# Optimization experiments

Hardware: AMD Instinct MI355X
Metric: run time of the kernel (lower is better)

The kernel has to match this reference:

```python
import jax, jax.numpy as jnp
import numpy as np

N = 100000
E = 1200000
F_IN = 128
HID = 32
HEADS = 4
OUT_HEADS = 1
N_CLASSES = 40
NEG_SLOPE = 0.2


def _glorot(key, shape):
    fan_in, fan_out = shape[0], shape[-1]
    lim = jnp.sqrt(6.0 / (fan_in + fan_out))
    return jax.random.uniform(key, shape, jnp.float32, -lim, lim)


def setup_inputs() -> dict:
    key = jax.random.key(0)
    ks = jax.random.split(key, 16)
    x = jax.random.normal(ks[0], (N, F_IN), jnp.float32)
    edge_index = jax.random.randint(ks[1], (2, E), 0, N, jnp.int32)
    # layer 0: F_IN -> HID per head, HEADS heads, concat
    W0 = _glorot(ks[2], (F_IN, HEADS * HID))
    a_src0 = _glorot(ks[3], (HEADS, HID))
    a_dst0 = _glorot(ks[4], (HEADS, HID))
    b0 = jnp.zeros((HEADS * HID,), jnp.float32)
    # layer 1: HEADS*HID -> HID per head, HEADS heads, concat
    W1 = _glorot(ks[5], (HEADS * HID, HEADS * HID))
    a_src1 = _glorot(ks[6], (HEADS, HID))
    a_dst1 = _glorot(ks[7], (HEADS, HID))
    b1 = jnp.zeros((HEADS * HID,), jnp.float32)
    # layer 2: HEADS*HID -> N_CLASSES, OUT_HEADS heads, concat=False (mean)
    W2 = _glorot(ks[8], (HEADS * HID, OUT_HEADS * N_CLASSES))
    a_src2 = _glorot(ks[9], (OUT_HEADS, N_CLASSES))
    a_dst2 = _glorot(ks[10], (OUT_HEADS, N_CLASSES))
    b2 = jnp.zeros((N_CLASSES,), jnp.float32)
    return dict(x=x, edge_index=edge_index,
                W0=W0, a_src0=a_src0, a_dst0=a_dst0, b0=b0,
                W1=W1, a_src1=a_src1, a_dst1=a_dst1, b1=b1,
                W2=W2, a_src2=a_src2, a_dst2=a_dst2, b2=b2)


def gat_conv(x, src, dst, W, a_src, a_dst, b, heads, ch, concat):
    n = x.shape[0]
    h = (x @ W).reshape(n, heads, ch)                      # [N,H,C]
    # per-node attention logits for source/target roles
    s_src = jnp.einsum('nhc,hc->nh', h, a_src)             # [N,H]
    s_dst = jnp.einsum('nhc,hc->nh', h, a_dst)             # [N,H]
    e = jax.nn.leaky_relu(s_src[src] + s_dst[dst], NEG_SLOPE)  # [E,H]
    # segment softmax over incoming edges of each target node
    emax = jax.ops.segment_max(e, dst, num_segments=n)
    ex = jnp.exp(e - emax[dst])
    denom = jax.ops.segment_sum(ex, dst, num_segments=n)
    alpha = ex / (denom[dst] + 1e-16)                       # [E,H]
    msg = h[src] * alpha[:, :, None]                        # [E,H,C]
    out = jax.ops.segment_sum(msg, dst, num_segments=n)     # [N,H,C]
    out = out.reshape(n, heads * ch) if concat else out.mean(axis=1)
    return out + b


def reference(x, edge_index, W0, a_src0, a_dst0, b0, W1, a_src1, a_dst1, b1,
              W2, a_src2, a_dst2, b2):
    # add self loops (PyG GATConv default)
    loops = jnp.arange(N, dtype=edge_index.dtype)
    src = jnp.concatenate([edge_index[0], loops])
    dst = jnp.concatenate([edge_index[1], loops])
    h = jax.nn.elu(gat_conv(x, src, dst, W0, a_src0, a_dst0, b0, HEADS, HID, True))
    h = jax.nn.elu(gat_conv(h, src, dst, W1, a_src1, a_dst1, b1, HEADS, HID, True))
    h = gat_conv(h, src, dst, W2, a_src2, a_dst2, b2, OUT_HEADS, N_CLASSES, False)
    return jax.nn.log_softmax(h, axis=1)
```

## Files before the change

kernel.cpp:

```cpp
#include <hip/hip_runtime.h>
#include <hip/hip_bf16.h>

#define FIN   128
#define HEADS 4
#define HID   32
#define NCLS  40
#define NEG_SLOPE 0.2f

#define BKT_SH 10
#define BKT    1024
#define NB_MAX 128
#define TILE_E 8192

typedef __bf16 bf16x8 __attribute__((ext_vector_type(8)));
typedef float  f32x4  __attribute__((ext_vector_type(4)));

__device__ inline unsigned short bf16_rne(float f) {
    unsigned u = __float_as_uint(f);
    return (unsigned short)((u + 0x7fffu + ((u >> 16) & 1u)) >> 16);
}
__device__ inline float bf16_to_f(unsigned short h) {
    return __uint_as_float(((unsigned)h) << 16);
}

__device__ inline void packW_dev(const float* __restrict__ W, unsigned short* __restrict__ Bhi,
                                 unsigned short* __restrict__ Blo, int NO, int NC, int idx) {
    int i = idx & 7;
    int rest = idx >> 3;
    int l = rest & 63;
    int rest2 = rest >> 6;
    int c = rest2 % NC;
    int t = rest2 / NC;
    int k   = t * 32 + (l >> 4) * 8 + i;
    int col = c * 16 + (l & 15);
    float val = (col < NO) ? W[(size_t)k * NO + col] : 0.f;
    unsigned short hi = bf16_rne(val);
    unsigned short lo = bf16_rne(val - bf16_to_f(hi));
    Bhi[idx] = hi;
    Blo[idx] = lo;
}

__device__ inline void packS_dev(const float* __restrict__ W, const float* __restrict__ asrc,
                                 const float* __restrict__ adst, unsigned short* __restrict__ Shi,
                                 unsigned short* __restrict__ Slo, int NO, int HH, int CH, int idx) {
    int i = idx & 7;
    int l = (idx >> 3) & 63;
    int t = idx >> 9;
    int k = t * 32 + (l >> 4) * 8 + i;
    int j = l & 15;
    float val = 0.f;
    if (j < 2 * HH) {
        int h = (j < HH) ? j : j - HH;
        const float* av = (j < HH) ? (asrc + h * CH) : (adst + h * CH);
        const float* wr = W + (size_t)k * NO + h * CH;
        for (int c = 0; c < CH; ++c) val += wr[c] * av[c];
    }
    unsigned short hi = bf16_rne(val);
    unsigned short lo = bf16_rne(val - bf16_to_f(hi));
    Shi[idx] = hi;
    Slo[idx] = lo;
}

__global__ __launch_bounds__(256) void packAll_k(
        const float* __restrict__ W0, const float* __restrict__ W1, const float* __restrict__ W2,
        const float* __restrict__ as0, const float* __restrict__ ad0,
        const float* __restrict__ as1, const float* __restrict__ ad1,
        const float* __restrict__ as2, const float* __restrict__ ad2,
        unsigned short* __restrict__ Bhi0, unsigned short* __restrict__ Blo0,
        unsigned short* __restrict__ Bhi1, unsigned short* __restrict__ Blo1,
        unsigned short* __restrict__ Bhi2, unsigned short* __restrict__ Blo2,
        unsigned short* __restrict__ Shi0, unsigned short* __restrict__ Slo0,
        unsigned short* __restrict__ Shi1, unsigned short* __restrict__ Slo1,
        unsigned short* __restrict__ Shi2, unsigned short* __restrict__ Slo2,
        int* __restrict__ cnt1) {
    int gid = blockIdx.x * 256 + threadIdx.x;
    if      (gid < 16384) packW_dev(W0, Bhi0, Blo0, 128, 8, gid);
    else if (gid < 32768) packW_dev(W1, Bhi1, Blo1, 128, 8, gid - 16384);
    else if (gid < 38912) packW_dev(W2, Bhi2, Blo2, NCLS, 3, gid - 32768);
    else if (gid < 40960) packS_dev(W0, as0, ad0, Shi0, Slo0, 128, 4, HID, gid - 38912);
    else if (gid < 43008) packS_dev(W1, as1, ad1, Shi1, Slo1, 128, 4, HID, gid - 40960);
    else if (gid < 45056) packS_dev(W2, as2, ad2, Shi2, Slo2, NCLS, 1, NCLS, gid - 43008);
    else if (gid < 45056 + NB_MAX) cnt1[gid - 45056] = 0;
}

template<int NC, int HH>
__global__ __launch_bounds__(256) void gemm_fused_k(
        const float* __restrict__ X, const unsigned short* __restrict__ Bhi,
        const unsigned short* __restrict__ Blo, const unsigned short* __restrict__ Shi,
        const unsigned short* __restrict__ Slo, unsigned short* __restrict__ Hbf,
        float* __restrict__ ssrc, float* __restrict__ sdst, int n, int NO) {
    int wave = threadIdx.x >> 6;
    int lane = threadIdx.x & 63;
    int rowbase = (blockIdx.x * 4 + wave) * 32;
    if (rowbase >= n) return;
    int r0 = lane & 15, kg = lane >> 4;

    f32x4 acc[2][NC];
    f32x4 accS[2];
#pragma unroll
    for (int rt = 0; rt < 2; ++rt) {
        accS[rt] = f32x4{0.f, 0.f, 0.f, 0.f};
#pragma unroll
        for (int c = 0; c < NC; ++c) acc[rt][c] = f32x4{0.f, 0.f, 0.f, 0.f};
    }

    for (int t = 0; t < 4; ++t) {
        union U { unsigned short u[8]; bf16x8 v; };
        U ah[2], al[2];
#pragma unroll
        for (int rt = 0; rt < 2; ++rt) {
            int row = min(rowbase + rt * 16 + r0, n - 1);
            const float* xp = X + (size_t)row * 128 + t * 32 + kg * 8;
            float4 xa = *reinterpret_cast<const float4*>(xp);
            float4 xb = *reinterpret_cast<const float4*>(xp + 4);
            float f[8] = {xa.x, xa.y, xa.z, xa.w, xb.x, xb.y, xb.z, xb.w};
#pragma unroll
            for (int i = 0; i < 8; ++i) {
                unsigned short h = bf16_rne(f[i]);
                ah[rt].u[i] = h;
                al[rt].u[i] = bf16_rne(f[i] - bf16_to_f(h));
            }
        }
#pragma unroll
        for (int c = 0; c < NC; ++c) {
            size_t boff = (((size_t)t * NC + c) * 64 + lane) * 8;
            bf16x8 bh = *reinterpret_cast<const bf16x8*>(Bhi + boff);
            bf16x8 bl = *reinterpret_cast<const bf16x8*>(Blo + boff);
#pragma unroll
            for (int rt = 0; rt < 2; ++rt) {
                acc[rt][c] = __builtin_amdgcn_mfma_f32_16x16x32_bf16(ah[rt].v, bh, acc[rt][c], 0, 0, 0);
                acc[rt][c] = __builtin_amdgcn_mfma_f32_16x16x32_bf16(al[rt].v, bh, acc[rt][c], 0, 0, 0);
                acc[rt][c] = __builtin_amdgcn_mfma_f32_16x16x32_bf16(ah[rt].v, bl, acc[rt][c], 0, 0, 0);
            }
        }
        {
            size_t soff = ((size_t)t * 64 + lane) * 8;
            bf16x8 sh = *reinterpret_cast<const bf16x8*>(Shi + soff);
            bf16x8 sl = *reinterpret_cast<const bf16x8*>(Slo + soff);
#pragma unroll
            for (int rt = 0; rt < 2; ++rt) {
                accS[rt] = __builtin_amdgcn_mfma_f32_16x16x32_bf16(ah[rt].v, sh, accS[rt], 0, 0, 0);
                accS[rt] = __builtin_amdgcn_mfma_f32_16x16x32_bf16(al[rt].v, sh, accS[rt], 0, 0, 0);
                accS[rt] = __builtin_amdgcn_mfma_f32_16x16x32_bf16(ah[rt].v, sl, accS[rt], 0, 0, 0);
            }
        }
    }

#pragma unroll
    for (int rt = 0; rt < 2; ++rt)
#pragma unroll
        for (int r = 0; r < 4; ++r) {
            int row = rowbase + rt * 16 + kg * 4 + r;
            if (row >= n) continue;
            if (HH == 4) {
                if (r0 < 4)      ssrc[(size_t)row * 4 + r0]       = accS[rt][r];
                else if (r0 < 8) sdst[(size_t)row * 4 + (r0 - 4)] = accS[rt][r];
            } else {
                if (r0 == 0)      ssrc[row] = accS[rt][r];
                else if (r0 == 1) sdst[row] = accS[rt][r];
            }
#pragma unroll
            for (int c = 0; c < NC; ++c) {
                int col = c * 16 + r0;
                if (col < NO)
                    Hbf[(size_t)row * NO + col] = bf16_rne(acc[rt][c][r]);
            }
        }
}

template<int NC, int HH, bool SPLIT>
__global__ __launch_bounds__(256) void gemm_bf16s_k(
        const unsigned short* __restrict__ Xbf, const unsigned short* __restrict__ Bhi,
        const unsigned short* __restrict__ Blo, const unsigned short* __restrict__ Shi,
        const unsigned short* __restrict__ Slo, unsigned short* __restrict__ Hbf,
        unsigned short* __restrict__ H8,
        float* __restrict__ ssrc, float* __restrict__ sdst, int n, int NO) {
    int wave = threadIdx.x >> 6;
    int lane = threadIdx.x & 63;
    int rowbase = (blockIdx.x * 4 + wave) * 32;
    if (rowbase >= n) return;
    int r0 = lane & 15, kg = lane >> 4;

    f32x4 acc[2][NC];
    f32x4 accS[2];
#pragma unroll
    for (int rt = 0; rt < 2; ++rt) {
        accS[rt] = f32x4{0.f, 0.f, 0.f, 0.f};
#pragma unroll
        for (int c = 0; c < NC; ++c) acc[rt][c] = f32x4{0.f, 0.f, 0.f, 0.f};
    }

    for (int t = 0; t < 4; ++t) {
        bf16x8 av[2];
#pragma unroll
        for (int rt = 0; rt < 2; ++rt) {
            int row = min(rowbase + rt * 16 + r0, n - 1);
            av[rt] = *reinterpret_cast<const bf16x8*>(Xbf + (size_t)row * 128 + t * 32 + kg * 8);
        }
#pragma unroll
        for (int c = 0; c < NC; ++c) {
            size_t boff = (((size_t)t * NC + c) * 64 + lane) * 8;
            bf16x8 bh = *reinterpret_cast<const bf16x8*>(Bhi + boff);
            bf16x8 bl = *reinterpret_cast<const bf16x8*>(Blo + boff);
#pragma unroll
            for (int rt = 0; rt < 2; ++rt) {
                acc[rt][c] = __builtin_amdgcn_mfma_f32_16x16x32_bf16(av[rt], bh, acc[rt][c], 0, 0, 0);
                acc[rt][c] = __builtin_amdgcn_mfma_f32_16x16x32_bf16(av[rt], bl, acc[rt][c], 0, 0, 0);
            }
        }
        {
            size_t soff = ((size_t)t * 64 + lane) * 8;
            bf16x8 sh = *reinterpret_cast<const bf16x8*>(Shi + soff);
            bf16x8 sl = *reinterpret_cast<const bf16x8*>(Slo + soff);
#pragma unroll
            for (int rt = 0; rt < 2; ++rt) {
                accS[rt] = __builtin_amdgcn_mfma_f32_16x16x32_bf16(av[rt], sh, accS[rt], 0, 0, 0);
                accS[rt] = __builtin_amdgcn_mfma_f32_16x16x32_bf16(av[rt], sl, accS[rt], 0, 0, 0);
            }
        }
    }

#pragma unroll
    for (int rt = 0; rt < 2; ++rt)
#pragma unroll
        for (int r = 0; r < 4; ++r) {
            int row = rowbase + rt * 16 + kg * 4 + r;
            if (row >= n) continue;
            if (HH == 4) {
                if (r0 < 4)      ssrc[(size_t)row * 4 + r0]       = accS[rt][r];
                else if (r0 < 8) sdst[(size_t)row * 4 + (r0 - 4)] = accS[rt][r];
            } else {
                if (r0 == 0)      ssrc[row] = accS[rt][r];
                else if (r0 == 1) sdst[row] = accS[rt][r];
            }
#pragma unroll
            for (int c = 0; c < NC; ++c) {
                int col = c * 16 + r0;
                if (col < NO) {
                    unsigned short b = bf16_rne(acc[rt][c][r]);
                    if (!SPLIT) {
                        Hbf[(size_t)row * 128 + col] = b;
                    } else {
                        if (col < 32) Hbf[(size_t)row * 32 + col] = b;
                        else          H8[(size_t)row * 8 + (col - 32)] = b;
                    }
                }
            }
        }
}

__global__ __launch_bounds__(256) void histA_k(const int* __restrict__ ei, int E, int Etot,
                                               int nb, int* __restrict__ cnt1) {
    __shared__ int h[NB_MAX];
    for (int i = threadIdx.x; i < nb; i += 256) h[i] = 0;
    __syncthreads();
    int base = blockIdx.x * TILE_E;
    int lim = min(base + TILE_E, Etot);
    for (int e = base + threadIdx.x; e < lim; e += 256) {
        int d = (e < E) ? ei[E + e] : e - E;
        atomicAdd(&h[d >> BKT_SH], 1);
    }
    __syncthreads();
    for (int i = threadIdx.x; i < nb; i += 256)
        if (h[i]) atomicAdd(&cnt1[i], h[i]);
}

__global__ void scanB_k(const int* __restrict__ cnt1, int* __restrict__ bbase,
                        int* __restrict__ gcur1, int nb) {
    __shared__ int tmp[128];
    int l = threadIdx.x;
    int v = (l < nb) ? cnt1[l] : 0;
    tmp[l] = v;
    __syncthreads();
    for (int off = 1; off < 128; off <<= 1) {
        int t = (l >= off) ? tmp[l - off] : 0;
        __syncthreads();
        tmp[l] += t;
        __syncthreads();
    }
    if (l < nb) { int ex = tmp[l] - v; bbase[l] = ex; gcur1[l] = ex; }
    if (l == 0) bbase[nb] = tmp[127];
}

__global__ __launch_bounds__(256) void placeA_k(const int* __restrict__ ei, int E, int Etot,
                                                int nb, int* __restrict__ gcur1,
                                                unsigned* __restrict__ pairs) {
    __shared__ int h[NB_MAX];
    __shared__ int cur[NB_MAX];
    for (int i = threadIdx.x; i < nb; i += 256) h[i] = 0;
    __syncthreads();
    int base = blockIdx.x * TILE_E;
    int lim = min(base + TILE_E, Etot);
    for (int e = base + threadIdx.x; e < lim; e += 256) {
        int d = (e < E) ? ei[E + e] : e - E;
        atomicAdd(&h[d >> BKT_SH], 1);
    }
    __syncthreads();
    for (int i = threadIdx.x; i < nb; i += 256)
        cur[i] = h[i] ? atomicAdd(&gcur1[i], h[i]) : 0;
    __syncthreads();
    for (int e = base + threadIdx.x; e < lim; e += 256) {
        int s, d;
        if (e < E) { s = ei[e]; d = ei[E + e]; } else { s = d = e - E; }
        int p = atomicAdd(&cur[d >> BKT_SH], 1);
        pairs[p] = ((unsigned)s << BKT_SH) | (unsigned)(d & (BKT - 1));
    }
}

__global__ __launch_bounds__(256) void buildcsr_k(const unsigned* __restrict__ pairs,
                                                  const int* __restrict__ bbase,
                                                  int* __restrict__ rowptr,
                                                  int* __restrict__ cols,
                                                  int n, int etot) {
    __shared__ int cnt[BKT];
    __shared__ int part[256];
    int b = blockIdx.x;
    int d0 = b << BKT_SH;
    int nd = min(BKT, n - d0);
    int rbeg = bbase[b], rend = bbase[b + 1];
    for (int i = threadIdx.x; i < nd; i += 256) cnt[i] = 0;
    __syncthreads();
    for (int i = rbeg + threadIdx.x; i < rend; i += 256)
        atomicAdd(&cnt[pairs[i] & (BKT - 1)], 1);
    __syncthreads();

    int t = threadIdx.x;
    int i4 = t * 4;
    int myv[4];
    int s0 = 0;
#pragma unroll
    for (int j = 0; j < 4; ++j) { myv[j] = (i4 + j < nd) ? cnt[i4 + j] : 0; s0 += myv[j]; }
    part[t] = s0;
    __syncthreads();
    for (int off = 1; off < 256; off <<= 1) {
        int tv = (t >= off) ? part[t - off] : 0;
        __syncthreads();
        part[t] += tv;
        __syncthreads();
    }
    int run = rbeg + part[t] - s0;
#pragma unroll
    for (int j = 0; j < 4; ++j) {
        if (i4 + j < nd) {
            rowptr[d0 + i4 + j] = run;
            cnt[i4 + j] = run;
            run += myv[j];
        }
    }
    if (b == 0 && t == 0) rowptr[n] = etot;
    __syncthreads();
    for (int i = rbeg + threadIdx.x; i < rend; i += 256) {
        unsigned p = pairs[i];
        int pos = atomicAdd(&cnt[p & (BKT - 1)], 1);
        cols[pos] = (int)(p >> BKT_SH);
    }
}

__global__ __launch_bounds__(256) void gat128_k(
        const int* __restrict__ rp, const int* __restrict__ cols,
        const unsigned short* __restrict__ Hbf, const float* __restrict__ ssrc,
        const float* __restrict__ sdst, const float* __restrict__ bias,
        unsigned short* __restrict__ outbf, int n) {
    int d = (blockIdx.x * 256 + threadIdx.x) >> 4;
    if (d >= n) return;
    int l = threadIdx.x & 15;
    int head = l >> 2;
    int beg = rp[d], end = rp[d + 1];

    float sdh = sdst[(size_t)d * 4 + head];

    float4 a0 = {0.f, 0.f, 0.f, 0.f}, a1 = {0.f, 0.f, 0.f, 0.f};
    float4 c0 = {0.f, 0.f, 0.f, 0.f}, c1 = {0.f, 0.f, 0.f, 0.f};
    float den = 0.f;

    auto proc = [&](int i, float4& p0, float4& p1) {
        int s = cols[i];
        float v = ssrc[(size_t)s * 4 + head] + sdh;
        v = (v >= 0.f) ? v : NEG_SLOPE * v;
        float a = __expf(v);
        den += a;
        const unsigned short* hp = Hbf + (size_t)s * 128 + l * 8;
        uint4 q = *reinterpret_cast<const uint4*>(hp);
        p0.x += a * __uint_as_float(q.x << 16);
        p0.y += a * __uint_as_float(q.x & 0xffff0000u);
        p0.z += a * __uint_as_float(q.y << 16);
        p0.w += a * __uint_as_float(q.y & 0xffff0000u);
        p1.x += a * __uint_as_float(q.z << 16);
        p1.y += a * __uint_as_float(q.z & 0xffff0000u);
        p1.z += a * __uint_as_float(q.w << 16);
        p1.w += a * __uint_as_float(q.w & 0xffff0000u);
    };

    int i = beg;
    int rem = (end - beg) & 3;
    if (rem & 1) { proc(i, a0, a1); ++i; }
    if (rem & 2) { proc(i, a0, a1); proc(i + 1, c0, c1); i += 2; }
    for (; i < end; i += 4) {
        int s0 = cols[i], s1 = cols[i + 1], s2 = cols[i + 2], s3 = cols[i + 3];
        float w0 = ssrc[(size_t)s0 * 4 + head] + sdh;
        float w1 = ssrc[(size_t)s1 * 4 + head] + sdh;
        float w2 = ssrc[(size_t)s2 * 4 + head] + sdh;
        float w3 = ssrc[(size_t)s3 * 4 + head] + sdh;
        uint4 q0 = *reinterpret_cast<const uint4*>(Hbf + (size_t)s0 * 128 + l * 8);
        uint4 q1 = *reinterpret_cast<const uint4*>(Hbf + (size_t)s1 * 128 + l * 8);
        uint4 q2 = *reinterpret_cast<const uint4*>(Hbf + (size_t)s2 * 128 + l * 8);
        uint4 q3 = *reinterpret_cast<const uint4*>(Hbf + (size_t)s3 * 128 + l * 8);
        w0 = (w0 >= 0.f) ? w0 : NEG_SLOPE * w0;
        w1 = (w1 >= 0.f) ? w1 : NEG_SLOPE * w1;
        w2 = (w2 >= 0.f) ? w2 : NEG_SLOPE * w2;
        w3 = (w3 >= 0.f) ? w3 : NEG_SLOPE * w3;
        float e0 = __expf(w0), e1 = __expf(w1);
        float e2 = __expf(w2), e3 = __expf(w3);
        den += e0 + e1 + e2 + e3;
        a0.x += e0 * __uint_as_float(q0.x << 16);
        a0.y += e0 * __uint_as_float(q0.x & 0xffff0000u);
        a0.z += e0 * __uint_as_float(q0.y << 16);
        a0.w += e0 * __uint_as_float(q0.y & 0xffff0000u);
        a1.x += e0 * __uint_as_float(q0.z << 16);
        a1.y += e0 * __uint_as_float(q0.z & 0xffff0000u);
        a1.z += e0 * __uint_as_float(q0.w << 16);
        a1.w += e0 * __uint_as_float(q0.w & 0xffff0000u);
        c0.x += e1 * __uint_as_float(q1.x << 16);
        c0.y += e1 * __uint_as_float(q1.x & 0xffff0000u);
        c0.z += e1 * __uint_as_float(q1.y << 16);
        c0.w += e1 * __uint_as_float(q1.y & 0xffff0000u);
        c1.x += e1 * __uint_as_float(q1.z << 16);
        c1.y += e1 * __uint_as_float(q1.z & 0xffff0000u);
        c1.z += e1 * __uint_as_float(q1.w << 16);
        c1.w += e1 * __uint_as_float(q1.w & 0xffff0000u);
        a0.x += e2 * __uint_as_float(q2.x << 16);
        a0.y += e2 * __uint_as_float(q2.x & 0xffff0000u);
        a0.z += e2 * __uint_as_float(q2.y << 16);
        a0.w += e2 * __uint_as_float(q2.y & 0xffff0000u);
        a1.x += e2 * __uint_as_float(q2.z << 16);
        a1.y += e2 * __uint_as_float(q2.z & 0xffff0000u);
        a1.z += e2 * __uint_as_float(q2.w << 16);
        a1.w += e2 * __uint_as_float(q2.w & 0xffff0000u);
        c0.x += e3 * __uint_as_float(q3.x << 16);
        c0.y += e3 * __uint_as_float(q3.x & 0xffff0000u);
        c0.z += e3 * __uint_as_float(q3.y << 16);
        c0.w += e3 * __uint_as_float(q3.y & 0xffff0000u);
        c1.x += e3 * __uint_as_float(q3.z << 16);
        c1.y += e3 * __uint_as_float(q3.z & 0xffff0000u);
        c1.z += e3 * __uint_as_float(q3.w << 16);
        c1.w += e3 * __uint_as_float(q3.w & 0xffff0000u);
    }
    a0.x += c0.x; a0.y += c0.y; a0.z += c0.z; a0.w += c0.w;
    a1.x += c1.x; a1.y += c1.y; a1.z += c1.z; a1.w += c1.w;

    float r = 1.f / (den + 1e-16f);
    float4 b0 = *reinterpret_cast<const float4*>(bias + l * 8);
    float4 b1 = *reinterpret_cast<const float4*>(bias + l * 8 + 4);
    float4 v0, v1;
    v0.x = a0.x * r + b0.x; v0.y = a0.y * r + b0.y;
    v0.z = a0.z * r + b0.z; v0.w = a0.w * r + b0.w;
    v1.x = a1.x * r + b1.x; v1.y = a1.y * r + b1.y;
    v1.z = a1.z * r + b1.z; v1.w = a1.w * r + b1.w;
    v0.x = (v0.x > 0.f) ? v0.x : expm1f(v0.x);
    v0.y = (v0.y > 0.f) ? v0.y : expm1f(v0.y);
    v0.z = (v0.z > 0.f) ? v0.z : expm1f(v0.z);
    v0.w = (v0.w > 0.f) ? v0.w : expm1f(v0.w);
    v1.x = (v1.x > 0.f) ? v1.x : expm1f(v1.x);
    v1.y = (v1.y > 0.f) ? v1.y : expm1f(v1.y);
    v1.z = (v1.z > 0.f) ? v1.z : expm1f(v1.z);
    v1.w = (v1.w > 0.f) ? v1.w : expm1f(v1.w);

    uint4 u;
    u.x = (unsigned)bf16_rne(v0.x) | ((unsigned)bf16_rne(v0.y) << 16);
    u.y = (unsigned)bf16_rne(v0.z) | ((unsigned)bf16_rne(v0.w) << 16);
    u.z = (unsigned)bf16_rne(v1.x) | ((unsigned)bf16_rne(v1.y) << 16);
    u.w = (unsigned)bf16_rne(v1.z) | ((unsigned)bf16_rne(v1.w) << 16);
    *reinterpret_cast<uint4*>(outbf + (size_t)d * 128 + l * 8) = u;
}

__global__ __launch_bounds__(256) void gat40_k(
        const int* __restrict__ rp, const int* __restrict__ cols,
        const unsigned short* __restrict__ H32, const unsigned short* __restrict__ H8,
        const float* __restrict__ ssrc, const float* __restrict__ sdst,
        const float* __restrict__ b2, float* __restrict__ out, int n) {
    int d = (blockIdx.x * 256 + threadIdx.x) >> 4;
    if (d >= n) return;
    int l = threadIdx.x & 15;
    int beg = rp[d], end = rp[d + 1];
    float sd = sdst[d];

    bool lo32 = (l < 8);
    int o32 = l * 4;
    int o8  = ((l >= 8 && l < 10) ? (l - 8) : 0) * 4;

    float4 acc = {0.f, 0.f, 0.f, 0.f};
    float4 acc2 = {0.f, 0.f, 0.f, 0.f};
    float den = 0.f;

    auto proc = [&](int i, float4& p) {
        int s = cols[i];
        float v = ssrc[s] + sd;
        v = (v >= 0.f) ? v : NEG_SLOPE * v;
        float a = __expf(v);
        den += a;
        const unsigned short* hp = lo32 ? (H32 + (size_t)s * 32 + o32)
                                        : (H8  + (size_t)s * 8  + o8);
        uint2 q = *reinterpret_cast<const uint2*>(hp);
        p.x += a * __uint_as_float(q.x << 16);
        p.y += a * __uint_as_float(q.x & 0xffff0000u);
        p.z += a * __uint_as_float(q.y << 16);
        p.w += a * __uint_as_float(q.y & 0xffff0000u);
    };
    int i = beg;
    int rem = (end - beg) & 3;
    if (rem & 1) { proc(i, acc); ++i; }
    if (rem & 2) { proc(i, acc); proc(i + 1, acc2); i += 2; }
    for (; i < end; i += 4) {
        int s0 = cols[i], s1 = cols[i + 1], s2 = cols[i + 2], s3 = cols[i + 3];
        float w0 = ssrc[s0] + sd, w1 = ssrc[s1] + sd;
        float w2 = ssrc[s2] + sd, w3 = ssrc[s3] + sd;
        const unsigned short* p0 = lo32 ? (H32 + (size_t)s0 * 32 + o32) : (H8 + (size_t)s0 * 8 + o8);
        const unsigned short* p1 = lo32 ? (H32 + (size_t)s1 * 32 + o32) : (H8 + (size_t)s1 * 8 + o8);
        const unsigned short* p2 = lo32 ? (H32 + (size_t)s2 * 32 + o32) : (H8 + (size_t)s2 * 8 + o8);
        const unsigned short* p3 = lo32 ? (H32 + (size_t)s3 * 32 + o32) : (H8 + (size_t)s3 * 8 + o8);
        uint2 q0 = *reinterpret_cast<const uint2*>(p0);
        uint2 q1 = *reinterpret_cast<const uint2*>(p1);
        uint2 q2 = *reinterpret_cast<const uint2*>(p2);
        uint2 q3 = *reinterpret_cast<const uint2*>(p3);
        w0 = (w0 >= 0.f) ? w0 : NEG_SLOPE * w0;
        w1 = (w1 >= 0.f) ? w1 : NEG_SLOPE * w1;
        w2 = (w2 >= 0.f) ? w2 : NEG_SLOPE * w2;
        w3 = (w3 >= 0.f) ? w3 : NEG_SLOPE * w3;
        float e0 = __expf(w0), e1 = __expf(w1);
        float e2 = __expf(w2), e3 = __expf(w3);
        den += e0 + e1 + e2 + e3;
        acc.x += e0 * __uint_as_float(q0.x << 16);
        acc.y += e0 * __uint_as_float(q0.x & 0xffff0000u);
        acc.z += e0 * __uint_as_float(q0.y << 16);
        acc.w += e0 * __uint_as_float(q0.y & 0xffff0000u);
        acc2.x += e1 * __uint_as_float(q1.x << 16);
        acc2.y += e1 * __uint_as_float(q1.x & 0xffff0000u);
        acc2.z += e1 * __uint_as_float(q1.y << 16);
        acc2.w += e1 * __uint_as_float(q1.y & 0xffff0000u);
        acc.x += e2 * __uint_as_float(q2.x << 16);
        acc.y += e2 * __uint_as_float(q2.x & 0xffff0000u);
        acc.z += e2 * __uint_as_float(q2.y << 16);
        acc.w += e2 * __uint_as_float(q2.y & 0xffff0000u);
        acc2.x += e3 * __uint_as_float(q3.x << 16);
        acc2.y += e3 * __uint_as_float(q3.x & 0xffff0000u);
        acc2.z += e3 * __uint_as_float(q3.y << 16);
        acc2.w += e3 * __uint_as_float(q3.y & 0xffff0000u);
    }
    acc.x += acc2.x; acc.y += acc2.y; acc.z += acc2.z; acc.w += acc2.w;

    float r = 1.f / (den + 1e-16f);
    float4 v4 = {0.f, 0.f, 0.f, 0.f};
    float mm = -1e30f;
    if (l < 10) {
        float4 b = *reinterpret_cast<const float4*>(b2 + l * 4);
        v4.x = acc.x * r + b.x; v4.y = acc.y * r + b.y;
        v4.z = acc.z * r + b.z; v4.w = acc.w * r + b.w;
        mm = fmaxf(fmaxf(v4.x, v4.y), fmaxf(v4.z, v4.w));
    }
    for (int off = 8; off > 0; off >>= 1) mm = fmaxf(mm, __shfl_xor(mm, off, 16));
    float ss = 0.f;
    if (l < 10)
        ss = __expf(v4.x - mm) + __expf(v4.y - mm) + __expf(v4.z - mm) + __expf(v4.w - mm);
    for (int off = 8; off > 0; off >>= 1) ss += __shfl_xor(ss, off, 16);
    float lse = mm + logf(ss);
    if (l < 10) {
        float4 o;
        o.x = v4.x - lse; o.y = v4.y - lse; o.z = v4.z - lse; o.w = v4.w - lse;
        *reinterpret_cast<float4*>(out + (size_t)d * 40 + l * 4) = o;
    }
}

static inline dim3 g1(long t) { return dim3((unsigned)((t + 255) / 256)); }

extern "C" void kernel_launch(void* const* d_in, const int* in_sizes, int n_in,
                              void* d_out, int out_size, void* d_ws, size_t ws_size,
                              hipStream_t stream) {
    const float* x      = (const float*)d_in[0];
    const int*   ei     = (const int*)d_in[1];
    const float* W0     = (const float*)d_in[2];
    const float* a_src0 = (const float*)d_in[3];
    const float* a_dst0 = (const float*)d_in[4];
    const float* b0     = (const float*)d_in[5];
    const float* W1     = (const float*)d_in[6];
    const float* a_src1 = (const float*)d_in[7];
    const float* a_dst1 = (const float*)d_in[8];
    const float* b1     = (const float*)d_in[9];
    const float* W2     = (const float*)d_in[10];
    const float* a_src2 = (const float*)d_in[11];
    const float* a_dst2 = (const float*)d_in[12];
    const float* b2     = (const float*)d_in[13];

    const int N    = in_sizes[0] / FIN;
    const int E    = in_sizes[1] / 2;
    const int Etot = E + N;
    const int NB   = (N + BKT - 1) / BKT;

    float* ws = (float*)d_ws;
    size_t o = 0;
    unsigned short* Hbf = (unsigned short*)(ws + o); o += (size_t)N * FIN / 2;
    unsigned short* Obf = (unsigned short*)(ws + o); o += (size_t)N * FIN / 2;
    unsigned short* H8  = (unsigned short*)(ws + o); o += (size_t)N * 4;
    float* ssrcA = ws + o; o += (size_t)N * HEADS;
    float* sdstA = ws + o; o += (size_t)N * HEADS;
    float* ssrcB = ws + o; o += (size_t)N * HEADS;
    float* sdstB = ws + o; o += (size_t)N * HEADS;
    int* cnt1   = (int*)(ws + o); o += NB_MAX;
    int* bbase  = (int*)(ws + o); o += NB_MAX + 2;
    int* gcur1  = (int*)(ws + o); o += NB_MAX;
    int* rowptr = (int*)(ws + o); o += N + 1;
    int* cols   = (int*)(ws + o); o += Etot;
    unsigned* pairs = (unsigned*)(ws + o); o += Etot;
    unsigned short* Bhi0 = (unsigned short*)(ws + o); o += 4 * 8 * 64 * 8 / 2;
    unsigned short* Blo0 = (unsigned short*)(ws + o); o += 4 * 8 * 64 * 8 / 2;
    unsigned short* Bhi1 = (unsigned short*)(ws + o); o += 4 * 8 * 64 * 8 / 2;
    unsigned short* Blo1 = (unsigned short*)(ws + o); o += 4 * 8 * 64 * 8 / 2;
    unsigned short* Bhi2 = (unsigned short*)(ws + o); o += 4 * 3 * 64 * 8 / 2;
    unsigned short* Blo2 = (unsigned short*)(ws + o); o += 4 * 3 * 64 * 8 / 2;
    unsigned short* Shi0 = (unsigned short*)(ws + o); o += 4 * 64 * 8 / 2;
    unsigned short* Slo0 = (unsigned short*)(ws + o); o += 4 * 64 * 8 / 2;
    unsigned short* Shi1 = (unsigned short*)(ws + o); o += 4 * 64 * 8 / 2;
    unsigned short* Slo1 = (unsigned short*)(ws + o); o += 4 * 64 * 8 / 2;
    unsigned short* Shi2 = (unsigned short*)(ws + o); o += 4 * 64 * 8 / 2;
    unsigned short* Slo2 = (unsigned short*)(ws + o); o += 4 * 64 * 8 / 2;

    const int gemmBlocks = (N + 127) / 128;
    const int grpBlocks  = (N * 16 + 255) / 256;
    const int eTiles     = (Etot + TILE_E - 1) / TILE_E;

    packAll_k<<<g1(45056 + NB_MAX), 256, 0, stream>>>(
        W0, W1, W2, a_src0, a_dst0, a_src1, a_dst1, a_src2, a_dst2,
        Bhi0, Blo0, Bhi1, Blo1, Bhi2, Blo2,
        Shi0, Slo0, Shi1, Slo1, Shi2, Slo2, cnt1);
    histA_k<<<eTiles, 256, 0, stream>>>(ei, E, Etot, NB, cnt1);
    scanB_k<<<1, 128, 0, stream>>>(cnt1, bbase, gcur1, NB);
    placeA_k<<<eTiles, 256, 0, stream>>>(ei, E, Etot, NB, gcur1, pairs);
    buildcsr_k<<<NB, 256, 0, stream>>>(pairs, bbase, rowptr, cols, N, Etot);

    gemm_fused_k<8, 4><<<gemmBlocks, 256, 0, stream>>>(x, Bhi0, Blo0, Shi0, Slo0, Hbf, ssrcA, sdstA, N, 128);
    gat128_k<<<grpBlocks, 256, 0, stream>>>(rowptr, cols, Hbf, ssrcA, sdstA, b0, Obf, N);

    gemm_bf16s_k<8, 4, false><<<gemmBlocks, 256, 0, stream>>>(Obf, Bhi1, Blo1, Shi1, Slo1, Hbf, nullptr, ssrcB, sdstB, N, 128);
    gat128_k<<<grpBlocks, 256, 0, stream>>>(rowptr, cols, Hbf, ssrcB, sdstB, b1, Obf, N);

    gemm_bf16s_k<3, 1, true><<<gemmBlocks, 256, 0, stream>>>(Obf, Bhi2, Blo2, Shi2, Slo2, Hbf, H8, ssrcA, sdstA, N, NCLS);
    gat40_k<<<grpBlocks, 256, 0, stream>>>(rowptr, cols, Hbf, H8, ssrcA, sdstA, b2, (float*)d_out, N);
}
```

Before: 311.7 us.

## Drop histogram pass with fixed-capacity buckets and degree-sort destination nodes

New measurement: 928.9 us. 2.98x slower.

```diff
diff --git a/kernel.cpp b/kernel.cpp
--- a/kernel.cpp
+++ b/kernel.cpp
@@ -11,6 +11,8 @@
 #define BKT    1024
 #define NB_MAX 128
 #define TILE_E 8192
+#define CAP_SH 14
+#define CAP    16384
 
 typedef __bf16 bf16x8 __attribute__((ext_vector_type(8)));
 typedef float  f32x4  __attribute__((ext_vector_type(4)));
@@ -72,7 +74,7 @@
         unsigned short* __restrict__ Shi0, unsigned short* __restrict__ Slo0,
         unsigned short* __restrict__ Shi1, unsigned short* __restrict__ Slo1,
         unsigned short* __restrict__ Shi2, unsigned short* __restrict__ Slo2,
-        int* __restrict__ cnt1) {
+        int* __restrict__ gcur1, int* __restrict__ degcnt) {
     int gid = blockIdx.x * 256 + threadIdx.x;
     if      (gid < 16384) packW_dev(W0, Bhi0, Blo0, 128, 8, gid);
     else if (gid < 32768) packW_dev(W1, Bhi1, Blo1, 128, 8, gid - 16384);
@@ -80,7 +82,8 @@
     else if (gid < 40960) packS_dev(W0, as0, ad0, Shi0, Slo0, 128, 4, HID, gid - 38912);
     else if (gid < 43008) packS_dev(W1, as1, ad1, Shi1, Slo1, 128, 4, HID, gid - 40960);
     else if (gid < 45056) packS_dev(W2, as2, ad2, Shi2, Slo2, NCLS, 1, NCLS, gid - 43008);
-    else if (gid < 45056 + NB_MAX) cnt1[gid - 45056] = 0;
+    else if (gid < 45056 + NB_MAX) gcur1[gid - 45056] = (gid - 45056) << CAP_SH;
+    else if (gid < 45056 + NB_MAX + 256) degcnt[gid - 45056 - NB_MAX] = 0;
 }
 
 template<int NC, int HH>
@@ -249,39 +252,6 @@
         }
 }
 
-__global__ __launch_bounds__(256) void histA_k(const int* __restrict__ ei, int E, int Etot,
-                                               int nb, int* __restrict__ cnt1) {
-    __shared__ int h[NB_MAX];
-    for (int i = threadIdx.x; i < nb; i += 256) h[i] = 0;
-    __syncthreads();
-    int base = blockIdx.x * TILE_E;
-    int lim = min(base + TILE_E, Etot);
-    for (int e = base + threadIdx.x; e < lim; e += 256) {
-        int d = (e < E) ? ei[E + e] : e - E;
-        atomicAdd(&h[d >> BKT_SH], 1);
-    }
-    __syncthreads();
-    for (int i = threadIdx.x; i < nb; i += 256)
-        if (h[i]) atomicAdd(&cnt1[i], h[i]);
-}
-
-__global__ void scanB_k(const int* __restrict__ cnt1, int* __restrict__ bbase,
-                        int* __restrict__ gcur1, int nb) {
-    __shared__ int tmp[128];
-    int l = threadIdx.x;
-    int v = (l < nb) ? cnt1[l] : 0;
-    tmp[l] = v;
-    __syncthreads();
-    for (int off = 1; off < 128; off <<= 1) {
-        int t = (l >= off) ? tmp[l - off] : 0;
-        __syncthreads();
-        tmp[l] += t;
-        __syncthreads();
-    }
-    if (l < nb) { int ex = tmp[l] - v; bbase[l] = ex; gcur1[l] = ex; }
-    if (l == 0) bbase[nb] = tmp[127];
-}
-
 __global__ __launch_bounds__(256) void placeA_k(const int* __restrict__ ei, int E, int Etot,
                                                 int nb, int* __restrict__ gcur1,
                                                 unsigned* __restrict__ pairs) {
@@ -302,25 +272,28 @@
     for (int e = base + threadIdx.x; e < lim; e += 256) {
         int s, d;
         if (e < E) { s = ei[e]; d = ei[E + e]; } else { s = d = e - E; }
-        int p = atomicAdd(&cur[d >> BKT_SH], 1);
-        pairs[p] = ((unsigned)s << BKT_SH) | (unsigned)(d & (BKT - 1));
+        int b = d >> BKT_SH;
+        int p = atomicAdd(&cur[b], 1);
+        if (p < ((b + 1) << CAP_SH))
+            pairs[p] = ((unsigned)s << BKT_SH) | (unsigned)(d & (BKT - 1));
     }
 }
 
 __global__ __launch_bounds__(256) void buildcsr_k(const unsigned* __restrict__ pairs,
-                                                  const int* __restrict__ bbase,
-                                                  int* __restrict__ rowptr,
-                                                  int* __restrict__ cols,
-                                                  int n, int etot) {
+                                                  const int* __restrict__ gcur1,
+                                                  int* __restrict__ begA, int* __restrict__ endA,
+                                                  int* __restrict__ cols, int* __restrict__ degcnt,
+                                                  int n) {
     __shared__ int cnt[BKT];
     __shared__ int part[256];
     int b = blockIdx.x;
+    int base = b << CAP_SH;
     int d0 = b << BKT_SH;
     int nd = min(BKT, n - d0);
-    int rbeg = bbase[b], rend = bbase[b + 1];
+    int total = min(gcur1[b] - base, CAP);
     for (int i = threadIdx.x; i < nd; i += 256) cnt[i] = 0;
     __syncthreads();
-    for (int i = rbeg + threadIdx.x; i < rend; i += 256)
+    for (int i = base + threadIdx.x; i < base + total; i += 256)
         atomicAdd(&cnt[pairs[i] & (BKT - 1)], 1);
     __syncthreads();
 
@@ -338,34 +311,62 @@
         part[t] += tv;
         __syncthreads();
     }
-    int run = rbeg + part[t] - s0;
+    int run = base + part[t] - s0;
 #pragma unroll
     for (int j = 0; j < 4; ++j) {
         if (i4 + j < nd) {
-            rowptr[d0 + i4 + j] = run;
+            begA[d0 + i4 + j] = run;
+            endA[d0 + i4 + j] = run + myv[j];
+            atomicAdd(&degcnt[min(myv[j], 255)], 1);
             cnt[i4 + j] = run;
             run += myv[j];
         }
     }
-    if (b == 0 && t == 0) rowptr[n] = etot;
-    __syncthreads();
-    for (int i = rbeg + threadIdx.x; i < rend; i += 256) {
+    __syncthreads();
+    for (int i = base + threadIdx.x; i < base + total; i += 256) {
         unsigned p = pairs[i];
         int pos = atomicAdd(&cnt[p & (BKT - 1)], 1);
         cols[pos] = (int)(p >> BKT_SH);
     }
 }
 
+__global__ void scanDeg_k(const int* __restrict__ degcnt, int* __restrict__ degcur) {
+    __shared__ int tmp[256];
+    int l = threadIdx.x;
+    int v = degcnt[l];
+    tmp[l] = v;
+    __syncthreads();
+    for (int off = 1; off < 256; off <<= 1) {
+        int t = (l >= off) ? tmp[l - off] : 0;
+        __syncthreads();
+        tmp[l] += t;
+        __syncthreads();
+    }
+    degcur[l] = tmp[l] - v;
+}
+
+__global__ __launch_bounds__(256) void permScatter_k(const int* __restrict__ begA,
+                                                     const int* __restrict__ endA,
+                                                     int* __restrict__ degcur,
+                                                     int* __restrict__ perm, int n) {
+    int d = blockIdx.x * 256 + threadIdx.x;
+    if (d >= n) return;
+    int deg = endA[d] - begA[d];
+    int pos = atomicAdd(&degcur[min(deg, 255)], 1);
+    perm[pos] = d;
+}
+
 __global__ __launch_bounds__(256) void gat128_k(
-        const int* __restrict__ rp, const int* __restrict__ cols,
-        const unsigned short* __restrict__ Hbf, const float* __restrict__ ssrc,
-        const float* __restrict__ sdst, const float* __restrict__ bias,
-        unsigned short* __restrict__ outbf, int n) {
-    int d = (blockIdx.x * 256 + threadIdx.x) >> 4;
-    if (d >= n) return;
+        const int* __restrict__ perm, const int* __restrict__ begA, const int* __restrict__ endA,
+        const int* __restrict__ cols, const unsigned short* __restrict__ Hbf,
+        const float* __restrict__ ssrc, const float* __restrict__ sdst,
+        const float* __restrict__ bias, unsigned short* __restrict__ outbf, int n) {
+    int g = (blockIdx.x * 256 + threadIdx.x) >> 4;
+    if (g >= n) return;
+    int d = perm[g];
     int l = threadIdx.x & 15;
     int head = l >> 2;
-    int beg = rp[d], end = rp[d + 1];
+    int beg = begA[d], end = endA[d];
 
     float sdh = sdst[(size_t)d * 4 + head];
 
@@ -474,14 +475,16 @@
 }
 
 __global__ __launch_bounds__(256) void gat40_k(
-        const int* __restrict__ rp, const int* __restrict__ cols,
-        const unsigned short* __restrict__ H32, const unsigned short* __restrict__ H8,
-        const float* __restrict__ ssrc, const float* __restrict__ sdst,
-        const float* __restrict__ b2, float* __restrict__ out, int n) {
-    int d = (blockIdx.x * 256 + threadIdx.x) >> 4;
-    if (d >= n) return;
+        const int* __restrict__ perm, const int* __restrict__ begA, const int* __restrict__ endA,
+        const int* __restrict__ cols, const unsigned short* __restrict__ H32,
+        const unsigned short* __restrict__ H8, const float* __restrict__ ssrc,
+        const float* __restrict__ sdst, const float* __restrict__ b2,
+        float* __restrict__ out, int n) {
+    int g = (blockIdx.x * 256 + threadIdx.x) >> 4;
+    if (g >= n) return;
+    int d = perm[g];
     int l = threadIdx.x & 15;
-    int beg = rp[d], end = rp[d + 1];
+    int beg = begA[d], end = endA[d];
     float sd = sdst[d];
 
     bool lo32 = (l < 8);
@@ -604,12 +607,14 @@
     float* sdstA = ws + o; o += (size_t)N * HEADS;
     float* ssrcB = ws + o; o += (size_t)N * HEADS;
     float* sdstB = ws + o; o += (size_t)N * HEADS;
-    int* cnt1   = (int*)(ws + o); o += NB_MAX;
-    int* bbase  = (int*)(ws + o); o += NB_MAX + 2;
     int* gcur1  = (int*)(ws + o); o += NB_MAX;
-    int* rowptr = (int*)(ws + o); o += N + 1;
-    int* cols   = (int*)(ws + o); o += Etot;
-    unsigned* pairs = (unsigned*)(ws + o); o += Etot;
+    int* degcnt = (int*)(ws + o); o += 256;
+    int* degcur = (int*)(ws + o); o += 256;
+    int* begA   = (int*)(ws + o); o += N;
+    int* endA   = (int*)(ws + o); o += N;
+    int* perm   = (int*)(ws + o); o += N;
+    int* cols   = (int*)(ws + o); o += (size_t)NB_MAX * CAP;
+    unsigned* pairs = (unsigned*)(ws + o); o += (size_t)NB_MAX * CAP;
     unsigned short* Bhi0 = (unsigned short*)(ws + o); o += 4 * 8 * 64 * 8 / 2;
     unsigned short* Blo0 = (unsigned short*)(ws + o); o += 4 * 8 * 64 * 8 / 2;
     unsigned short* Bhi1 = (unsigned short*)(ws + o); o += 4 * 8 * 64 * 8 / 2;
@@ -627,21 +632,21 @@
     const int grpBlocks  = (N * 16 + 255) / 256;
     const int eTiles     = (Etot + TILE_E - 1) / TILE_E;
 
-    packAll_k<<<g1(45056 + NB_MAX), 256, 0, stream>>>(
+    packAll_k<<<g1(45056 + NB_MAX + 256), 256, 0, stream>>>(
         W0, W1, W2, a_src0, a_dst0, a_src1, a_dst1, a_src2, a_dst2,
         Bhi0, Blo0, Bhi1, Blo1, Bhi2, Blo2,
-        Shi0, Slo0, Shi1, Slo1, Shi2, Slo2, cnt1);
-    histA_k<<<eTiles, 256, 0, stream>>>(ei, E, Etot, NB, cnt1);
-    scanB_k<<<1, 128, 0, stream>>>(cnt1, bbase, gcur1, NB);
+        Shi0, Slo0, Shi1, Slo1, Shi2, Slo2, gcur1, degcnt);
     placeA_k<<<eTiles, 256, 0, stream>>>(ei, E, Etot, NB, gcur1, pairs);
-    buildcsr_k<<<NB, 256, 0, stream>>>(pairs, bbase, rowptr, cols, N, Etot);
+    buildcsr_k<<<NB, 256, 0, stream>>>(pairs, gcur1, begA, endA, cols, degcnt, N);
+    scanDeg_k<<<1, 256, 0, stream>>>(degcnt, degcur);
+    permScatter_k<<<g1(N), 256, 0, stream>>>(begA, endA, degcur, perm, N);
 
     gemm_fused_k<8, 4><<<gemmBlocks, 256, 0, stream>>>(x, Bhi0, Blo0, Shi0, Slo0, Hbf, ssrcA, sdstA, N, 128);
-    gat128_k<<<grpBlocks, 256, 0, stream>>>(rowptr, cols, Hbf, ssrcA, sdstA, b0, Obf, N);
+    gat128_k<<<grpBlocks, 256, 0, stream>>>(perm, begA, endA, cols, Hbf, ssrcA, sdstA, b0, Obf, N);
 
     gemm_bf16s_k<8, 4, false><<<gemmBlocks, 256, 0, stream>>>(Obf, Bhi1, Blo1, Shi1, Slo1, Hbf, nullptr, ssrcB, sdstB, N, 128);
-    gat128_k<<<grpBlocks, 256, 0, stream>>>(rowptr, cols, Hbf, ssrcB, sdstB, b1, Obf, N);
+    gat128_k<<<grpBlocks, 256, 0, stream>>>(perm, begA, endA, cols, Hbf, ssrcB, sdstB, b1, Obf, N);
 
     gemm_bf16s_k<3, 1, true><<<gemmBlocks, 256, 0, stream>>>(Obf, Bhi2, Blo2, Shi2, Slo2, Hbf, H8, ssrcA, sdstA, N, NCLS);
-    gat40_k<<<grpBlocks, 256, 0, stream>>>(rowptr, cols, Hbf, H8, ssrcA, sdstA, b2, (float*)d_out, N);
-}
+    gat40_k<<<grpBlocks, 256, 0, stream>>>(perm, begA, endA, cols, Hbf, H8, ssrcA, sdstA, b2, (float*)d_out, N);
+}
```
